# Kernel optimization log

Hardware: AMD Instinct MI355X
Metric: run time of the kernel (lower is better)

## Reference

```python
import jax, jax.numpy as jnp
import numpy as np

N, E, G = 50000, 640000, 1024
D, RD, H = 128, 200, 512
NUM_ATOM_FEATS, ATOM_VOCAB = 9, 64
NUM_BOND_FEATS, BOND_VOCAB = 3, 16


def setup_inputs() -> dict:
    key = jax.random.key(0)
    ks = jax.random.split(key, 24)
    inp = {
        "x_feat": jax.random.randint(ks[0], (N, NUM_ATOM_FEATS), 0, ATOM_VOCAB),
        "edge_index": jax.random.randint(ks[1], (2, E), 0, N),
        "edge_attr_feat": jax.random.randint(ks[2], (E, NUM_BOND_FEATS), 0, BOND_VOCAB),
        "batch": jnp.sort(jax.random.randint(ks[3], (N,), 0, G)),
        "rdkit_feats": jax.random.normal(ks[4], (G, RD), dtype=jnp.float32),
        # learned params
        "atom_emb": jax.random.normal(ks[5], (NUM_ATOM_FEATS, ATOM_VOCAB, D), dtype=jnp.float32) * 0.02,
        "bond_emb": jax.random.normal(ks[6], (NUM_BOND_FEATS, BOND_VOCAB, D), dtype=jnp.float32) * 0.02,
        "conv1_w1": jax.random.normal(ks[7], (D, D), dtype=jnp.float32) / np.sqrt(D),
        "conv1_b1": jnp.zeros((D,), jnp.float32),
        "conv1_w2": jax.random.normal(ks[8], (D, D), dtype=jnp.float32) / np.sqrt(D),
        "conv1_b2": jnp.zeros((D,), jnp.float32),
        "conv2_w1": jax.random.normal(ks[9], (D, D), dtype=jnp.float32) / np.sqrt(D),
        "conv2_b1": jnp.zeros((D,), jnp.float32),
        "conv2_w2": jax.random.normal(ks[10], (D, D), dtype=jnp.float32) / np.sqrt(D),
        "conv2_b2": jnp.zeros((D,), jnp.float32),
        "mlp_w1": jax.random.normal(ks[11], (D + RD, H), dtype=jnp.float32) / np.sqrt(D + RD),
        "mlp_b1": jnp.zeros((H,), jnp.float32),
        "mlp_w2": jax.random.normal(ks[12], (H, H // 2), dtype=jnp.float32) / np.sqrt(H),
        "mlp_b2": jnp.zeros((H // 2,), jnp.float32),
        "mlp_w3": jax.random.normal(ks[13], (H // 2, 1), dtype=jnp.float32) / np.sqrt(H // 2),
        "mlp_b3": jnp.zeros((1,), jnp.float32),
    }
    return inp


def _gine_conv(x, edge_index, edge_attr, w1, b1, w2, b2, eps=0.0):
    # PyG GINEConv: out = nn((1+eps)*x + sum_{j in N(i)} relu(x_j + e_ji))
    src, dst = edge_index[0], edge_index[1]
    msg = jax.nn.relu(x[src] + edge_attr)               # [E, D]
    agg = jax.ops.segment_sum(msg, dst, num_segments=x.shape[0])  # [N, D]
    h = (1.0 + eps) * x + agg
    h = jax.nn.relu(h @ w1 + b1)
    return h @ w2 + b2


def reference(x_feat, edge_index, edge_attr_feat, batch, rdkit_feats,
              atom_emb, bond_emb,
              conv1_w1, conv1_b1, conv1_w2, conv1_b2,
              conv2_w1, conv2_b1, conv2_w2, conv2_b2,
              mlp_w1, mlp_b1, mlp_w2, mlp_b2, mlp_w3, mlp_b3):
    # AtomEncoder / BondEncoder: sum of per-feature categorical embeddings
    x = atom_emb[jnp.arange(NUM_ATOM_FEATS)[None, :], x_feat].sum(axis=1)          # [N, D]
    edge_attr = bond_emb[jnp.arange(NUM_BOND_FEATS)[None, :], edge_attr_feat].sum(axis=1)  # [E, D]

    x = _gine_conv(x, edge_index, edge_attr, conv1_w1, conv1_b1, conv1_w2, conv1_b2)
    x = _gine_conv(x, edge_index, edge_attr, conv2_w1, conv2_b1, conv2_w2, conv2_b2)

    # global mean pool over graphs
    sums = jax.ops.segment_sum(x, batch, num_segments=G)                # [G, D]
    counts = jax.ops.segment_sum(jnp.ones((x.shape[0],), x.dtype), batch, num_segments=G)
    pooled = sums / jnp.maximum(counts, 1.0)[:, None]

    h = jnp.concatenate([pooled, rdkit_feats], axis=1)                  # [G, D+RD]
    h = jax.nn.relu(h @ mlp_w1 + mlp_b1)   # dropout is identity in eval mode
    h = jax.nn.relu(h @ mlp_w2 + mlp_b2)
    return h @ mlp_w3 + mlp_b3                                          # [G, 1]
```

## Files before the change

kernel.cpp:

```cpp
#include <hip/hip_runtime.h>

#define N_NODES 50000
#define N_EDGES 640000
#define N_GRAPH 1024
#define D 128
#define RD 200

typedef __attribute__((ext_vector_type(4))) float f32x4;
typedef __attribute__((ext_vector_type(8))) float f32x8;
typedef __attribute__((ext_vector_type(4))) _Float16 half4;
typedef __attribute__((ext_vector_type(8))) _Float16 half8;

static __device__ __forceinline__ int lbound(const int* a, int n, int v) {
  int lo = 0, hi = n;
  while (lo < hi) { int m = (lo + hi) >> 1; if (a[m] < v) lo = m + 1; else hi = m; }
  return lo;
}

__global__ void k_prep(const float* __restrict__ w0, const float* __restrict__ w1,
                       const float* __restrict__ w2, const float* __restrict__ w3,
                       const float* __restrict__ mw1, const float* __restrict__ mw2,
                       const float* __restrict__ emb,
                       _Float16* __restrict__ cWf,
                       _Float16* __restrict__ W1f,
                       _Float16* __restrict__ W2f,
                       _Float16* __restrict__ embh,
                       int* __restrict__ deg) {
  int t = blockIdx.x * 256 + threadIdx.x;
  if (t < N_NODES) deg[t] = 0;
  if (t < 8192) {
    int mat = t >> 11, r = t & 2047;
    int frag = r >> 6, lane = r & 63;
    int n0 = frag >> 2, kk = frag & 3;
    int n = n0 * 16 + (lane & 15);
    int kb = (lane >> 4) * 8 + kk * 32;
    const float* W = (mat == 0) ? w0 : (mat == 1) ? w1 : (mat == 2) ? w2 : w3;
    half8 o;
#pragma unroll
    for (int j = 0; j < 8; ++j) o[j] = (_Float16)W[(kb + j) * D + n];
    *(half8*)&cWf[((size_t)mat * 2048 + r) * 8] = o;
  } else if (t < 8192 + 22528) {
    int u = t - 8192;
    int frag = u >> 6, lane = u & 63;
    int n0 = frag / 11, kk = frag % 11;
    int n = n0 * 16 + (lane & 15);
    int kb = (lane >> 4) * 8 + kk * 32;
    half8 o;
#pragma unroll
    for (int j = 0; j < 8; ++j) {
      int k = kb + j;
      o[j] = (k < 328) ? (_Float16)mw1[k * 512 + n] : (_Float16)0.f;
    }
    *(half8*)&W1f[(size_t)u * 8] = o;
  } else if (t < 8192 + 22528 + 16384) {
    int u = t - 8192 - 22528;
    int frag = u >> 6, lane = u & 63;
    int n0 = frag >> 4, kk = frag & 15;
    int n = n0 * 16 + (lane & 15);
    int kb = (lane >> 4) * 8 + kk * 32;
    half8 o;
#pragma unroll
    for (int j = 0; j < 8; ++j) o[j] = (_Float16)mw2[(kb + j) * 256 + n];
    *(half8*)&W2f[(size_t)u * 8] = o;
  } else if (t < 8192 + 22528 + 16384 + 9216) {
    int u = t - 8192 - 22528 - 16384;
    float4 v0 = *(const float4*)&emb[(size_t)u * 8];
    float4 v1 = *(const float4*)&emb[(size_t)u * 8 + 4];
    half8 o;
    o[0] = (_Float16)v0.x; o[1] = (_Float16)v0.y; o[2] = (_Float16)v0.z; o[3] = (_Float16)v0.w;
    o[4] = (_Float16)v1.x; o[5] = (_Float16)v1.y; o[6] = (_Float16)v1.z; o[7] = (_Float16)v1.w;
    *(half8*)&embh[(size_t)u * 8] = o;
  }
}

__global__ void k_atom_count(const int* __restrict__ xf, const _Float16* __restrict__ embh,
                             _Float16* __restrict__ x16,
                             const int* __restrict__ ei, const int* __restrict__ bondf,
                             int* __restrict__ deg,
                             int2* __restrict__ drep) {
  if (blockIdx.x < 3125) {
    int t = blockIdx.x * 256 + threadIdx.x;
    int node = t >> 4, c = (t & 15) << 3;
    int v[9];
#pragma unroll
    for (int f = 0; f < 9; ++f) v[f] = xf[node * 9 + f];
    f32x8 a = (f32x8)(0.f);
#pragma unroll
    for (int f = 0; f < 9; ++f) {
      half8 e8 = *(const half8*)&embh[(size_t)(f * 64 + v[f]) * D + c];
      a += __builtin_convertvector(e8, f32x8);
    }
    half8 o;
#pragma unroll
    for (int tt = 0; tt < 8; ++tt) o[tt] = (_Float16)a[tt];
    *(half8*)&x16[(size_t)node * D + c] = o;
  } else {
    int e = (blockIdx.x - 3125) * 256 + threadIdx.x;
    if (e < N_EDGES) {
      int d = ei[N_EDGES + e];
      int rank = atomicAdd(&deg[d], 1);
      int s = ei[e];
      int f0 = bondf[e * 3], f1 = bondf[e * 3 + 1], f2 = bondf[e * 3 + 2];
      drep[e] = make_int2(d | (rank << 16), s | (f0 << 16) | (f1 << 20) | (f2 << 24));
    }
  }
}

__global__ void k_scan_blocks(const int* __restrict__ deg, int* __restrict__ excl,
                              int* __restrict__ bsum) {
  __shared__ int sd[1024];
  int i = blockIdx.x * 1024 + threadIdx.x;
  int v = (i < N_NODES) ? deg[i] : 0;
  sd[threadIdx.x] = v;
  __syncthreads();
  for (int off = 1; off < 1024; off <<= 1) {
    int t = (threadIdx.x >= (unsigned)off) ? sd[threadIdx.x - off] : 0;
    __syncthreads();
    sd[threadIdx.x] += t;
    __syncthreads();
  }
  if (i < N_NODES) excl[i] = sd[threadIdx.x] - v;
  if (threadIdx.x == 1023) bsum[blockIdx.x] = sd[1023];
}

__global__ void k_scan_add(int* __restrict__ row_ptr, const int* __restrict__ bsum) {
  __shared__ int s_off;
  if (threadIdx.x < 64) {
    int v = ((int)threadIdx.x < (int)blockIdx.x) ? bsum[threadIdx.x] : 0;
#pragma unroll
    for (int o = 1; o < 64; o <<= 1) v += __shfl_xor(v, o);
    if (threadIdx.x == 0) s_off = v;
  }
  __syncthreads();
  int off = s_off;
  int i = blockIdx.x * 1024 + threadIdx.x;
  if (i < N_NODES) row_ptr[i] += off;
  if (blockIdx.x == 0 && threadIdx.x == 0) row_ptr[N_NODES] = N_EDGES;
}

__global__ void k_fill(const int2* __restrict__ drep,
                       const int* __restrict__ row_ptr, int* __restrict__ csr1) {
  int e = blockIdx.x * 256 + threadIdx.x;
  if (e >= N_EDGES) return;
  int2 v = drep[e];
  int d = v.x & 0xFFFF;
  int rank = ((unsigned)v.x) >> 16;
  csr1[row_ptr[d] + rank] = v.y;
}

__global__ __launch_bounds__(256) void k_agg(
    const _Float16* __restrict__ X, const int* __restrict__ row_ptr,
    const int* __restrict__ csr1, const float* __restrict__ bemb,
    _Float16* __restrict__ out) {
  __shared__ half8 sB[48 * 16];
  for (int t = threadIdx.x; t < 768; t += blockDim.x) {
    float4 v0 = *(const float4*)&bemb[t * 8];
    float4 v1 = *(const float4*)&bemb[t * 8 + 4];
    half8 h;
    h[0] = (_Float16)v0.x; h[1] = (_Float16)v0.y; h[2] = (_Float16)v0.z; h[3] = (_Float16)v0.w;
    h[4] = (_Float16)v1.x; h[5] = (_Float16)v1.y; h[6] = (_Float16)v1.z; h[7] = (_Float16)v1.w;
    sB[t] = h;
  }
  __syncthreads();
  int lane = threadIdx.x & 63;
  int quad = lane >> 4, l15 = lane & 15, c8 = l15 * 8;
  int wid = blockIdx.x * 4 + (threadIdx.x >> 6);
  int nw = gridDim.x * 4;
  for (int i = wid; i < N_NODES; i += nw) {
    int e0 = row_ptr[i], e1 = row_ptr[i + 1];
    int degn = e1 - e0;
    int dq = degn > 64 ? 64 : degn;
    int creg = (lane < dq) ? csr1[e0 + lane] : 0;
    f32x8 ac0 = (f32x8)(0.f), ac1 = (f32x8)(0.f);
    for (int jb = 0; jb < dq; jb += 8) {
      unsigned e0v = (unsigned)__shfl(creg, jb + quad);
      unsigned e1v = (unsigned)__shfl(creg, jb + 4 + quad);
      if (jb + quad < dq) {
        half8 x0 = *(const half8*)&X[(size_t)(e0v & 0xFFFF) * D + c8];
        unsigned p0 = e0v >> 16;
        half8 m0h = (x0 + sB[(p0 & 15) * 16 + l15]) +
                    (sB[256 + ((p0 >> 4) & 15) * 16 + l15] + sB[512 + (p0 >> 8) * 16 + l15]);
        f32x8 g0 = __builtin_convertvector(m0h, f32x8);
#pragma unroll
        for (int tt = 0; tt < 8; ++tt) ac0[tt] += fmaxf(g0[tt], 0.f);
      }
      if (jb + 4 + quad < dq) {
        half8 x1 = *(const half8*)&X[(size_t)(e1v & 0xFFFF) * D + c8];
        unsigned p1 = e1v >> 16;
        half8 m1h = (x1 + sB[(p1 & 15) * 16 + l15]) +
                    (sB[256 + ((p1 >> 4) & 15) * 16 + l15] + sB[512 + (p1 >> 8) * 16 + l15]);
        f32x8 g1 = __builtin_convertvector(m1h, f32x8);
#pragma unroll
        for (int tt = 0; tt < 8; ++tt) ac1[tt] += fmaxf(g1[tt], 0.f);
      }
    }
    for (int jj = e0 + 64 + quad; jj < e1; jj += 4) {
      unsigned ev = (unsigned)csr1[jj];
      half8 x0 = *(const half8*)&X[(size_t)(ev & 0xFFFF) * D + c8];
      unsigned p0 = ev >> 16;
      half8 m0h = (x0 + sB[(p0 & 15) * 16 + l15]) +
                  (sB[256 + ((p0 >> 4) & 15) * 16 + l15] + sB[512 + (p0 >> 8) * 16 + l15]);
      f32x8 g0 = __builtin_convertvector(m0h, f32x8);
#pragma unroll
      for (int tt = 0; tt < 8; ++tt) ac0[tt] += fmaxf(g0[tt], 0.f);
    }
    f32x8 acc = ac0 + ac1;
#pragma unroll
    for (int tt = 0; tt < 8; ++tt) {
      acc[tt] += __shfl_xor(acc[tt], 16);
      acc[tt] += __shfl_xor(acc[tt], 32);
    }
    if (quad == 0) {
      half8 sr = *(const half8*)&X[(size_t)i * D + c8];
      f32x8 o = __builtin_convertvector(sr, f32x8) + acc;
      half8 oh;
#pragma unroll
      for (int tt = 0; tt < 8; ++tt) oh[tt] = (_Float16)o[tt];
      *(half8*)&out[(size_t)i * D + c8] = oh;
    }
  }
}

__global__ __launch_bounds__(256) void k_conv(
    const _Float16* __restrict__ A,
    const _Float16* __restrict__ W1f, const float* __restrict__ b1,
    const _Float16* __restrict__ W2f, const float* __restrict__ b2,
    _Float16* __restrict__ O16) {
  __shared__ _Float16 sW[2048 * 8];
  __shared__ _Float16 sI[128 * 136];
  int tid = threadIdx.x, w = tid >> 6, lane = tid & 63;
  int m0 = blockIdx.x * 128;
  int col16 = lane & 15, q = lane >> 4;
  for (int t = tid; t < 2048; t += 256)
    *(float4*)&sW[t * 8] = *(const float4*)&W1f[(size_t)t * 8];
  half8 afr[2][4];
#pragma unroll
  for (int f = 0; f < 2; ++f) {
    int row = m0 + w * 32 + f * 16 + col16;
    if (row >= N_NODES) row = N_NODES - 1;
    const _Float16* Ar = A + (size_t)row * D + q * 8;
#pragma unroll
    for (int kk = 0; kk < 4; ++kk) afr[f][kk] = *(const half8*)(Ar + kk * 32);
  }
  __syncthreads();
#pragma unroll
  for (int n0 = 0; n0 < 8; ++n0) {
    f32x4 a0 = {0.f, 0.f, 0.f, 0.f}, a1 = {0.f, 0.f, 0.f, 0.f};
#pragma unroll
    for (int kk = 0; kk < 4; ++kk) {
      half8 b = *(const half8*)&sW[((n0 * 4 + kk) * 64 + lane) * 8];
      a0 = __builtin_amdgcn_mfma_f32_16x16x32_f16(afr[0][kk], b, a0, 0, 0, 0);
      a1 = __builtin_amdgcn_mfma_f32_16x16x32_f16(afr[1][kk], b, a1, 0, 0, 0);
    }
    float bb = b1[n0 * 16 + col16];
#pragma unroll
    for (int r = 0; r < 4; ++r) {
      sI[(w * 32 + q * 4 + r) * 136 + n0 * 16 + col16] = (_Float16)fmaxf(a0[r] + bb, 0.f);
      sI[(w * 32 + 16 + q * 4 + r) * 136 + n0 * 16 + col16] = (_Float16)fmaxf(a1[r] + bb, 0.f);
    }
  }
  __syncthreads();
  for (int t = tid; t < 2048; t += 256)
    *(float4*)&sW[t * 8] = *(const float4*)&W2f[(size_t)t * 8];
  half8 a2[2][4];
#pragma unroll
  for (int f = 0; f < 2; ++f) {
    const _Float16* tr = &sI[(w * 32 + f * 16 + col16) * 136 + q * 8];
#pragma unroll
    for (int kk = 0; kk < 4; ++kk) a2[f][kk] = *(const half8*)(tr + kk * 32);
  }
  __syncthreads();
#pragma unroll
  for (int n0 = 0; n0 < 8; ++n0) {
    f32x4 a0 = {0.f, 0.f, 0.f, 0.f}, a1 = {0.f, 0.f, 0.f, 0.f};
#pragma unroll
    for (int kk = 0; kk < 4; ++kk) {
      half8 b = *(const half8*)&sW[((n0 * 4 + kk) * 64 + lane) * 8];
      a0 = __builtin_amdgcn_mfma_f32_16x16x32_f16(a2[0][kk], b, a0, 0, 0, 0);
      a1 = __builtin_amdgcn_mfma_f32_16x16x32_f16(a2[1][kk], b, a1, 0, 0, 0);
    }
    int col = n0 * 16 + col16;
    float bb = b2[col];
#pragma unroll
    for (int r = 0; r < 4; ++r) {
      int r0 = m0 + w * 32 + q * 4 + r;
      int r1 = r0 + 16;
      if (r0 < N_NODES) O16[(size_t)r0 * D + col] = (_Float16)(a0[r] + bb);
      if (r1 < N_NODES) O16[(size_t)r1 * D + col] = (_Float16)(a1[r] + bb);
    }
  }
}

__global__ __launch_bounds__(256) void k_pool(
    const _Float16* __restrict__ x, const int* __restrict__ batch,
    const float* __restrict__ rdkit, _Float16* __restrict__ hcat,
    const float* __restrict__ B3, float* __restrict__ out) {
  int g = blockIdx.x * 4 + (threadIdx.x >> 6);
  if (g >= N_GRAPH) return;
  int lane = threadIdx.x & 63;
  int half_ = lane >> 5;
  int c4 = (lane & 31) * 4;
  int lo = lbound(batch, N_NODES, g);
  int hi = lbound(batch, N_NODES, g + 1);
  f32x4 a = {0.f, 0.f, 0.f, 0.f};
  for (int i = lo + half_; i < hi; i += 2) {
    half4 v = *(const half4*)&x[(size_t)i * D + c4];
    a += __builtin_convertvector(v, f32x4);
  }
#pragma unroll
  for (int t = 0; t < 4; ++t) a[t] += __shfl_xor(a[t], 32);
  float inv = 1.f / fmaxf((float)(hi - lo), 1.f);
  if (half_ == 0) {
    half4 o;
    o.x = (_Float16)(a[0] * inv); o.y = (_Float16)(a[1] * inv);
    o.z = (_Float16)(a[2] * inv); o.w = (_Float16)(a[3] * inv);
    *(half4*)&hcat[(size_t)g * 352 + c4] = o;
  }
  for (int r = lane; r < RD; r += 64)
    hcat[(size_t)g * 352 + D + r] = (_Float16)rdkit[(size_t)g * RD + r];
  if (lane < 24) hcat[(size_t)g * 352 + 328 + lane] = (_Float16)0.f;
  if (lane == 0) out[g] = B3[0];
}

__global__ __launch_bounds__(256) void k_mlp1(
    const _Float16* __restrict__ A, const _Float16* __restrict__ W1f,
    const float* __restrict__ B, _Float16* __restrict__ O) {
  int w = threadIdx.x >> 6, lane = threadIdx.x & 63;
  int gid = blockIdx.x * 4 + w;
  int mt = gid >> 5, n0 = gid & 31;
  int col16 = lane & 15, q = lane >> 4;
  const _Float16* Ar = A + (size_t)(mt * 16 + col16) * 352 + q * 8;
  f32x4 acc = {0.f, 0.f, 0.f, 0.f};
#pragma unroll
  for (int kk = 0; kk < 11; ++kk) {
    half8 a = *(const half8*)(Ar + kk * 32);
    half8 b = *(const half8*)&W1f[(size_t)((n0 * 11 + kk) * 64 + lane) * 8];
    acc = __builtin_amdgcn_mfma_f32_16x16x32_f16(a, b, acc, 0, 0, 0);
  }
  int col = n0 * 16 + col16;
  float bb = B[col];
#pragma unroll
  for (int r = 0; r < 4; ++r) {
    int row = mt * 16 + q * 4 + r;
    O[(size_t)row * 512 + col] = (_Float16)fmaxf(acc[r] + bb, 0.f);
  }
}

__global__ __launch_bounds__(256) void k_mlp23(
    const _Float16* __restrict__ A, const _Float16* __restrict__ W2f,
    const float* __restrict__ B2, const float* __restrict__ W3,
    float* __restrict__ out) {
  int w = threadIdx.x >> 6, lane = threadIdx.x & 63;
  int gid = blockIdx.x * 4 + w;
  int mt = gid >> 4, n0 = gid & 15;
  int col16 = lane & 15, q = lane >> 4;
  const _Float16* Ar = A + (size_t)(mt * 16 + col16) * 512 + q * 8;
  f32x4 acc = {0.f, 0.f, 0.f, 0.f};
#pragma unroll
  for (int kk = 0; kk < 16; ++kk) {
    half8 a = *(const half8*)(Ar + kk * 32);
    half8 b = *(const half8*)&W2f[(size_t)((n0 * 16 + kk) * 64 + lane) * 8];
    acc = __builtin_amdgcn_mfma_f32_16x16x32_f16(a, b, acc, 0, 0, 0);
  }
  int col = n0 * 16 + col16;
  float bb = B2[col], w3 = W3[col];
  float p[4];
#pragma unroll
  for (int r = 0; r < 4; ++r) p[r] = fmaxf(acc[r] + bb, 0.f) * w3;
#pragma unroll
  for (int r = 0; r < 4; ++r) {
    p[r] += __shfl_xor(p[r], 1);
    p[r] += __shfl_xor(p[r], 2);
    p[r] += __shfl_xor(p[r], 4);
    p[r] += __shfl_xor(p[r], 8);
  }
  if (col16 == 0) {
#pragma unroll
    for (int r = 0; r < 4; ++r)
      atomicAdd(&out[mt * 16 + q * 4 + r], p[r]);
  }
}

extern "C" void kernel_launch(void* const* d_in, const int* in_sizes, int n_in,
                              void* d_out, int out_size, void* d_ws, size_t ws_size,
                              hipStream_t stream) {
  const int* x_feat = (const int*)d_in[0];
  const int* ei = (const int*)d_in[1];
  const int* bondf = (const int*)d_in[2];
  const int* batch = (const int*)d_in[3];
  const float* rdkit = (const float*)d_in[4];
  const float* atom_emb = (const float*)d_in[5];
  const float* bond_emb = (const float*)d_in[6];
  const float* c1w1 = (const float*)d_in[7];
  const float* c1b1 = (const float*)d_in[8];
  const float* c1w2 = (const float*)d_in[9];
  const float* c1b2 = (const float*)d_in[10];
  const float* c2w1 = (const float*)d_in[11];
  const float* c2b1 = (const float*)d_in[12];
  const float* c2w2 = (const float*)d_in[13];
  const float* c2b2 = (const float*)d_in[14];
  const float* mw1 = (const float*)d_in[15];
  const float* mb1 = (const float*)d_in[16];
  const float* mw2 = (const float*)d_in[17];
  const float* mb2 = (const float*)d_in[18];
  const float* mw3 = (const float*)d_in[19];
  const float* mb3 = (const float*)d_in[20];
  float* out = (float*)d_out;

  char* ws = (char*)d_ws;
  size_t off = 0;
  auto alloc = [&](size_t bytes) {
    void* p = ws + off;
    off += (bytes + 255) & ~(size_t)255;
    return p;
  };
  _Float16* x16a = (_Float16*)alloc((size_t)N_NODES * D * 2);
  _Float16* x16b = (_Float16*)alloc((size_t)N_NODES * D * 2);
  _Float16* h16 = (_Float16*)alloc((size_t)N_NODES * D * 2);
  _Float16* x2_16 = (_Float16*)alloc((size_t)N_NODES * D * 2);
  int* deg = (int*)alloc((size_t)N_NODES * 4);
  int* row_ptr = (int*)alloc((size_t)(N_NODES + 1) * 4);
  int* bsum = (int*)alloc(64 * 4);
  int* csr1 = (int*)alloc((size_t)N_EDGES * 4);
  int2* drep = (int2*)alloc((size_t)N_EDGES * 8);
  _Float16* hcat16 = (_Float16*)alloc((size_t)N_GRAPH * 352 * 2);
  _Float16* h1buf = (_Float16*)alloc((size_t)N_GRAPH * 512 * 2);
  _Float16* cWf = (_Float16*)alloc((size_t)4 * 2048 * 8 * 2);
  _Float16* W1f = (_Float16*)alloc((size_t)352 * 64 * 8 * 2);
  _Float16* W2f = (_Float16*)alloc((size_t)256 * 64 * 8 * 2);
  _Float16* embh = (_Float16*)alloc((size_t)9 * 64 * D * 2);

  k_prep<<<256, 256, 0, stream>>>(c1w1, c1w2, c2w1, c2w2, mw1, mw2, atom_emb,
                                  cWf, W1f, W2f, embh, deg);
  k_atom_count<<<3125 + 2500, 256, 0, stream>>>(x_feat, embh, x16a,
                                                ei, bondf, deg, drep);

  int nb = (N_NODES + 1023) / 1024;
  k_scan_blocks<<<nb, 1024, 0, stream>>>(deg, row_ptr, bsum);
  k_scan_add<<<nb, 1024, 0, stream>>>(row_ptr, bsum);
  k_fill<<<(N_EDGES + 255) / 256, 256, 0, stream>>>(drep, row_ptr, csr1);

  int ctiles = (N_NODES + 127) / 128;
  k_agg<<<2048, 256, 0, stream>>>(x16a, row_ptr, csr1, bond_emb, h16);
  k_conv<<<ctiles, 256, 0, stream>>>(h16, cWf + 0 * 16384, c1b1,
                                     cWf + 1 * 16384, c1b2, x16b);
  k_agg<<<2048, 256, 0, stream>>>(x16b, row_ptr, csr1, bond_emb, h16);
  k_conv<<<ctiles, 256, 0, stream>>>(h16, cWf + 2 * 16384, c2b1,
                                     cWf + 3 * 16384, c2b2, x2_16);

  k_pool<<<N_GRAPH / 4, 256, 0, stream>>>(x2_16, batch, rdkit, hcat16, mb3, out);
  k_mlp1<<<512, 256, 0, stream>>>(hcat16, W1f, mb1, h1buf);
  k_mlp23<<<256, 256, 0, stream>>>(h1buf, W2f, mb2, mw3, out);

  (void)in_sizes; (void)n_in; (void)out_size; (void)ws_size;
}
```

Baseline: 280.3 us.

## Fuse pooling and MLP head into one kernel; single-block degree scan

Replaces the two-kernel block scan with a single 1024-thread block where each thread scans 49 consecutive degrees serially. Merges mean-pool, MLP layer 1 and layers 2/3 into one kernel that keeps the concatenated features and hidden activations in shared memory, handling 16 graphs per block. This removes several kernel launches and global round-trips for intermediates. In exchange, the head kernel runs only 64 blocks with more serial work per wave, and the scan's strided loads are uncoalesced.

```diff
diff --git a/kernel.cpp b/kernel.cpp
--- a/kernel.cpp
+++ b/kernel.cpp
@@ -106,36 +106,36 @@
   }
 }
 
-__global__ void k_scan_blocks(const int* __restrict__ deg, int* __restrict__ excl,
-                              int* __restrict__ bsum) {
+__global__ __launch_bounds__(1024) void k_scan1(const int* __restrict__ deg,
+                                                int* __restrict__ row_ptr) {
   __shared__ int sd[1024];
-  int i = blockIdx.x * 1024 + threadIdx.x;
-  int v = (i < N_NODES) ? deg[i] : 0;
-  sd[threadIdx.x] = v;
+  int t = threadIdx.x;
+  int base = t * 49;
+  int v[49];
+  int s = 0;
+#pragma unroll
+  for (int j = 0; j < 49; ++j) {
+    int i = base + j;
+    int d = (i < N_NODES) ? deg[i] : 0;
+    v[j] = d;
+    s += d;
+  }
+  sd[t] = s;
   __syncthreads();
   for (int off = 1; off < 1024; off <<= 1) {
-    int t = (threadIdx.x >= (unsigned)off) ? sd[threadIdx.x - off] : 0;
+    int x = (t >= off) ? sd[t - off] : 0;
     __syncthreads();
-    sd[threadIdx.x] += t;
+    sd[t] += x;
     __syncthreads();
   }
-  if (i < N_NODES) excl[i] = sd[threadIdx.x] - v;
-  if (threadIdx.x == 1023) bsum[blockIdx.x] = sd[1023];
-}
-
-__global__ void k_scan_add(int* __restrict__ row_ptr, const int* __restrict__ bsum) {
-  __shared__ int s_off;
-  if (threadIdx.x < 64) {
-    int v = ((int)threadIdx.x < (int)blockIdx.x) ? bsum[threadIdx.x] : 0;
-#pragma unroll
-    for (int o = 1; o < 64; o <<= 1) v += __shfl_xor(v, o);
-    if (threadIdx.x == 0) s_off = v;
-  }
-  __syncthreads();
-  int off = s_off;
-  int i = blockIdx.x * 1024 + threadIdx.x;
-  if (i < N_NODES) row_ptr[i] += off;
-  if (blockIdx.x == 0 && threadIdx.x == 0) row_ptr[N_NODES] = N_EDGES;
+  int run = sd[t] - s;
+#pragma unroll
+  for (int j = 0; j < 49; ++j) {
+    int i = base + j;
+    if (i < N_NODES) row_ptr[i] = run;
+    run += v[j];
+  }
+  if (t == 0) row_ptr[N_NODES] = N_EDGES;
 }
 
 __global__ void k_fill(const int2* __restrict__ drep,
@@ -291,93 +291,105 @@
   }
 }
 
-__global__ __launch_bounds__(256) void k_pool(
+__global__ __launch_bounds__(256) void k_head(
     const _Float16* __restrict__ x, const int* __restrict__ batch,
-    const float* __restrict__ rdkit, _Float16* __restrict__ hcat,
-    const float* __restrict__ B3, float* __restrict__ out) {
-  int g = blockIdx.x * 4 + (threadIdx.x >> 6);
-  if (g >= N_GRAPH) return;
-  int lane = threadIdx.x & 63;
-  int half_ = lane >> 5;
-  int c4 = (lane & 31) * 4;
-  int lo = lbound(batch, N_NODES, g);
-  int hi = lbound(batch, N_NODES, g + 1);
-  f32x4 a = {0.f, 0.f, 0.f, 0.f};
-  for (int i = lo + half_; i < hi; i += 2) {
-    half4 v = *(const half4*)&x[(size_t)i * D + c4];
-    a += __builtin_convertvector(v, f32x4);
-  }
-#pragma unroll
-  for (int t = 0; t < 4; ++t) a[t] += __shfl_xor(a[t], 32);
-  float inv = 1.f / fmaxf((float)(hi - lo), 1.f);
-  if (half_ == 0) {
-    half4 o;
-    o.x = (_Float16)(a[0] * inv); o.y = (_Float16)(a[1] * inv);
-    o.z = (_Float16)(a[2] * inv); o.w = (_Float16)(a[3] * inv);
-    *(half4*)&hcat[(size_t)g * 352 + c4] = o;
-  }
-  for (int r = lane; r < RD; r += 64)
-    hcat[(size_t)g * 352 + D + r] = (_Float16)rdkit[(size_t)g * RD + r];
-  if (lane < 24) hcat[(size_t)g * 352 + 328 + lane] = (_Float16)0.f;
-  if (lane == 0) out[g] = B3[0];
-}
-
-__global__ __launch_bounds__(256) void k_mlp1(
-    const _Float16* __restrict__ A, const _Float16* __restrict__ W1f,
-    const float* __restrict__ B, _Float16* __restrict__ O) {
-  int w = threadIdx.x >> 6, lane = threadIdx.x & 63;
-  int gid = blockIdx.x * 4 + w;
-  int mt = gid >> 5, n0 = gid & 31;
+    const float* __restrict__ rdkit,
+    const _Float16* __restrict__ W1f, const float* __restrict__ B1,
+    const _Float16* __restrict__ W2f, const float* __restrict__ B2,
+    const float* __restrict__ W3, const float* __restrict__ B3,
+    float* __restrict__ out) {
+  __shared__ _Float16 sH[16 * 360];
+  __shared__ _Float16 sH1[16 * 520];
+  int tid = threadIdx.x, w = tid >> 6, lane = tid & 63;
+  int g0 = blockIdx.x * 16;
   int col16 = lane & 15, q = lane >> 4;
-  const _Float16* Ar = A + (size_t)(mt * 16 + col16) * 352 + q * 8;
-  f32x4 acc = {0.f, 0.f, 0.f, 0.f};
-#pragma unroll
-  for (int kk = 0; kk < 11; ++kk) {
-    half8 a = *(const half8*)(Ar + kk * 32);
-    half8 b = *(const half8*)&W1f[(size_t)((n0 * 11 + kk) * 64 + lane) * 8];
-    acc = __builtin_amdgcn_mfma_f32_16x16x32_f16(a, b, acc, 0, 0, 0);
-  }
-  int col = n0 * 16 + col16;
-  float bb = B[col];
-#pragma unroll
-  for (int r = 0; r < 4; ++r) {
-    int row = mt * 16 + q * 4 + r;
-    O[(size_t)row * 512 + col] = (_Float16)fmaxf(acc[r] + bb, 0.f);
-  }
-}
-
-__global__ __launch_bounds__(256) void k_mlp23(
-    const _Float16* __restrict__ A, const _Float16* __restrict__ W2f,
-    const float* __restrict__ B2, const float* __restrict__ W3,
-    float* __restrict__ out) {
-  int w = threadIdx.x >> 6, lane = threadIdx.x & 63;
-  int gid = blockIdx.x * 4 + w;
-  int mt = gid >> 4, n0 = gid & 15;
-  int col16 = lane & 15, q = lane >> 4;
-  const _Float16* Ar = A + (size_t)(mt * 16 + col16) * 512 + q * 8;
-  f32x4 acc = {0.f, 0.f, 0.f, 0.f};
-#pragma unroll
-  for (int kk = 0; kk < 16; ++kk) {
-    half8 a = *(const half8*)(Ar + kk * 32);
-    half8 b = *(const half8*)&W2f[(size_t)((n0 * 16 + kk) * 64 + lane) * 8];
-    acc = __builtin_amdgcn_mfma_f32_16x16x32_f16(a, b, acc, 0, 0, 0);
-  }
-  int col = n0 * 16 + col16;
-  float bb = B2[col], w3 = W3[col];
-  float p[4];
-#pragma unroll
-  for (int r = 0; r < 4; ++r) p[r] = fmaxf(acc[r] + bb, 0.f) * w3;
-#pragma unroll
-  for (int r = 0; r < 4; ++r) {
-    p[r] += __shfl_xor(p[r], 1);
-    p[r] += __shfl_xor(p[r], 2);
-    p[r] += __shfl_xor(p[r], 4);
-    p[r] += __shfl_xor(p[r], 8);
-  }
-  if (col16 == 0) {
-#pragma unroll
-    for (int r = 0; r < 4; ++r)
-      atomicAdd(&out[mt * 16 + q * 4 + r], p[r]);
+
+  {
+    int half_ = lane >> 5;
+    int c4 = (lane & 31) * 4;
+#pragma unroll
+    for (int gg = 0; gg < 4; ++gg) {
+      int row = w * 4 + gg;
+      int g = g0 + row;
+      int lo = lbound(batch, N_NODES, g);
+      int hi = lbound(batch, N_NODES, g + 1);
+      f32x4 a = {0.f, 0.f, 0.f, 0.f};
+      for (int i = lo + half_; i < hi; i += 2) {
+        half4 v = *(const half4*)&x[(size_t)i * D + c4];
+        a += __builtin_convertvector(v, f32x4);
+      }
+#pragma unroll
+      for (int t = 0; t < 4; ++t) a[t] += __shfl_xor(a[t], 32);
+      float inv = 1.f / fmaxf((float)(hi - lo), 1.f);
+      if (half_ == 0) {
+        half4 o;
+        o.x = (_Float16)(a[0] * inv); o.y = (_Float16)(a[1] * inv);
+        o.z = (_Float16)(a[2] * inv); o.w = (_Float16)(a[3] * inv);
+        *(half4*)&sH[row * 360 + c4] = o;
+      }
+      for (int r = lane; r < RD; r += 64)
+        sH[row * 360 + 128 + r] = (_Float16)rdkit[(size_t)g * RD + r];
+      if (lane < 32) sH[row * 360 + 328 + lane] = (_Float16)0.f;
+      if (lane == 0) out[g] = B3[0];
+    }
+  }
+  __syncthreads();
+
+  {
+    half8 afr[11];
+    const _Float16* Ar = &sH[col16 * 360 + q * 8];
+#pragma unroll
+    for (int kk = 0; kk < 11; ++kk) afr[kk] = *(const half8*)(Ar + kk * 32);
+#pragma unroll
+    for (int ng = 0; ng < 8; ++ng) {
+      int n0 = w * 8 + ng;
+      f32x4 acc = {0.f, 0.f, 0.f, 0.f};
+#pragma unroll
+      for (int kk = 0; kk < 11; ++kk) {
+        half8 b = *(const half8*)&W1f[(size_t)((n0 * 11 + kk) * 64 + lane) * 8];
+        acc = __builtin_amdgcn_mfma_f32_16x16x32_f16(afr[kk], b, acc, 0, 0, 0);
+      }
+      int col = n0 * 16 + col16;
+      float bb = B1[col];
+#pragma unroll
+      for (int r = 0; r < 4; ++r)
+        sH1[(q * 4 + r) * 520 + col] = (_Float16)fmaxf(acc[r] + bb, 0.f);
+    }
+  }
+  __syncthreads();
+
+  {
+    half8 a2[16];
+    const _Float16* Ar = &sH1[col16 * 520 + q * 8];
+#pragma unroll
+    for (int kk = 0; kk < 16; ++kk) a2[kk] = *(const half8*)(Ar + kk * 32);
+    float p[4] = {0.f, 0.f, 0.f, 0.f};
+#pragma unroll
+    for (int ng = 0; ng < 4; ++ng) {
+      int n0 = w * 4 + ng;
+      f32x4 acc = {0.f, 0.f, 0.f, 0.f};
+#pragma unroll
+      for (int kk = 0; kk < 16; ++kk) {
+        half8 b = *(const half8*)&W2f[(size_t)((n0 * 16 + kk) * 64 + lane) * 8];
+        acc = __builtin_amdgcn_mfma_f32_16x16x32_f16(a2[kk], b, acc, 0, 0, 0);
+      }
+      int col = n0 * 16 + col16;
+      float bb = B2[col], w3 = W3[col];
+#pragma unroll
+      for (int r = 0; r < 4; ++r) p[r] += fmaxf(acc[r] + bb, 0.f) * w3;
+    }
+#pragma unroll
+    for (int r = 0; r < 4; ++r) {
+      p[r] += __shfl_xor(p[r], 1);
+      p[r] += __shfl_xor(p[r], 2);
+      p[r] += __shfl_xor(p[r], 4);
+      p[r] += __shfl_xor(p[r], 8);
+    }
+    if (col16 == 0) {
+#pragma unroll
+      for (int r = 0; r < 4; ++r)
+        atomicAdd(&out[g0 + q * 4 + r], p[r]);
+    }
   }
 }
 
@@ -420,11 +432,8 @@
   _Float16* x2_16 = (_Float16*)alloc((size_t)N_NODES * D * 2);
   int* deg = (int*)alloc((size_t)N_NODES * 4);
   int* row_ptr = (int*)alloc((size_t)(N_NODES + 1) * 4);
-  int* bsum = (int*)alloc(64 * 4);
   int* csr1 = (int*)alloc((size_t)N_EDGES * 4);
   int2* drep = (int2*)alloc((size_t)N_EDGES * 8);
-  _Float16* hcat16 = (_Float16*)alloc((size_t)N_GRAPH * 352 * 2);
-  _Float16* h1buf = (_Float16*)alloc((size_t)N_GRAPH * 512 * 2);
   _Float16* cWf = (_Float16*)alloc((size_t)4 * 2048 * 8 * 2);
   _Float16* W1f = (_Float16*)alloc((size_t)352 * 64 * 8 * 2);
   _Float16* W2f = (_Float16*)alloc((size_t)256 * 64 * 8 * 2);
@@ -434,10 +443,7 @@
                                   cWf, W1f, W2f, embh, deg);
   k_atom_count<<<3125 + 2500, 256, 0, stream>>>(x_feat, embh, x16a,
                                                 ei, bondf, deg, drep);
-
-  int nb = (N_NODES + 1023) / 1024;
-  k_scan_blocks<<<nb, 1024, 0, stream>>>(deg, row_ptr, bsum);
-  k_scan_add<<<nb, 1024, 0, stream>>>(row_ptr, bsum);
+  k_scan1<<<1, 1024, 0, stream>>>(deg, row_ptr);
   k_fill<<<(N_EDGES + 255) / 256, 256, 0, stream>>>(drep, row_ptr, csr1);
 
   int ctiles = (N_NODES + 127) / 128;
@@ -448,9 +454,8 @@
   k_conv<<<ctiles, 256, 0, stream>>>(h16, cWf + 2 * 16384, c2b1,
                                      cWf + 3 * 16384, c2b2, x2_16);
 
-  k_pool<<<N_GRAPH / 4, 256, 0, stream>>>(x2_16, batch, rdkit, hcat16, mb3, out);
-  k_mlp1<<<512, 256, 0, stream>>>(hcat16, W1f, mb1, h1buf);
-  k_mlp23<<<256, 256, 0, stream>>>(h1buf, W2f, mb2, mw3, out);
+  k_head<<<N_GRAPH / 16, 256, 0, stream>>>(x2_16, batch, rdkit,
+                                           W1f, mb1, W2f, mb2, mw3, mb3, out);
 
   (void)in_sizes; (void)n_in; (void)out_size; (void)ws_size;
 }
```

New measurement: 402.4 us. +43.6%, slower.
